# Performance work log

Measured on AMD Instinct MI355X. Metric: run time of the kernel, lower is better.

## Reference

```python
import jax, jax.numpy as jnp
import numpy as np
import math

B, N = 1, 768
CS, CZ, CH, H, PQ, PV = 384, 128, 16, 12, 4, 8
EPS = 1e-8


def setup_inputs() -> dict:
    key = jax.random.key(0)
    ks = jax.random.split(key, 12)
    def rn(k, shape, scale=1.0):
        return jax.random.normal(k, shape, dtype=jnp.float32) * scale
    s = rn(ks[0], (B, N, CS))
    z = rn(ks[1], (B, N, N, CZ))
    rot, _ = jnp.linalg.qr(rn(ks[2], (B, N, 3, 3)))  # proper-ish rigid rotations
    rot = rot.astype(jnp.float32)
    trans = rn(ks[3], (B, N, 3))
    sc = 0.02
    Wq = rn(ks[4], (CS, H * CH), sc); bq = jnp.zeros((H * CH,), jnp.float32)
    Wkv = rn(ks[5], (CS, 2 * H * CH), sc); bkv = jnp.zeros((2 * H * CH,), jnp.float32)
    Wqp = rn(ks[6], (CS, H * PQ * 3), sc); bqp = jnp.zeros((H * PQ * 3,), jnp.float32)
    Wkvp = rn(ks[7], (CS, H * (PQ + PV) * 3), sc); bkvp = jnp.zeros((H * (PQ + PV) * 3,), jnp.float32)
    Wb = rn(ks[8], (CZ, H), sc); bb = jnp.zeros((H,), jnp.float32)
    head_w = rn(ks[9], (H,), 0.5)
    Wout = rn(ks[10], (H * (CZ + CH + PV * 4), CS), sc); bout = jnp.zeros((CS,), jnp.float32)
    return dict(s=s, z=z, rot=rot, trans=trans, Wq=Wq, bq=bq, Wkv=Wkv, bkv=bkv,
                Wqp=Wqp, bqp=bqp, Wkvp=Wkvp, bkvp=bkvp, Wb=Wb, bb=bb,
                head_w=head_w, Wout=Wout, bout=bout)


def _split_points(x):
    # [B,N,3*M] -> [B,N,M,3]: first M entries are x-coords, next M y, next M z
    return jnp.stack(jnp.split(x, 3, axis=-1), axis=-1)


def _apply_frame(rot, trans, pts):
    # pts [B,N,M,3] -> R @ p + t
    return jnp.einsum('bnxy,bnmy->bnmx', rot, pts) + trans[:, :, None, :]


def reference(s, z, rot, trans, Wq, bq, Wkv, bkv, Wqp, bqp, Wkvp, bkvp, Wb, bb, head_w, Wout, bout):
    # scalar q/k/v: [B,N,H,CH]
    q = (s @ Wq + bq).reshape(B, N, H, CH)
    kv = (s @ Wkv + bkv).reshape(B, N, H, 2 * CH)
    k, v = kv[..., :CH], kv[..., CH:]

    # point q/k/v in global frame
    q_pts = _apply_frame(rot, trans, _split_points(s @ Wqp + bqp)).reshape(B, N, H, PQ, 3)
    kv_pts = _apply_frame(rot, trans, _split_points(s @ Wkvp + bkvp)).reshape(B, N, H, PQ + PV, 3)
    k_pts, v_pts = kv_pts[..., :PQ, :], kv_pts[..., PQ:, :]

    # pair bias [B,N,N,H]
    b = z @ Wb + bb

    # scalar attention logits [B,H,i,j]
    a = jnp.einsum('bihc,bjhc->bhij', q, k) * math.sqrt(1.0 / (3 * CH))
    a = a + math.sqrt(1.0 / 3) * jnp.transpose(b, (0, 3, 1, 2))

    # point-distance attention: [B,i,j,H,PQ]
    diff = q_pts[:, :, None] - k_pts[:, None]          # [B,i,j,H,PQ,3]
    d2 = jnp.sum(diff * diff, axis=-1)                  # [B,i,j,H,PQ]
    hw = jax.nn.softplus(head_w) * math.sqrt(1.0 / (3 * (PQ * 9.0 / 2)))
    pt_att = -0.5 * jnp.sum(d2 * hw[None, None, None, :, None], axis=-1)  # [B,i,j,H]
    a = a + jnp.transpose(pt_att, (0, 3, 1, 2))

    a = jax.nn.softmax(a, axis=-1)                      # [B,H,i,j]

    # scalar output [B,N,H*CH]
    o = jnp.einsum('bhij,bjhc->bihc', a, v).reshape(B, N, H * CH)

    # point output [B,i,H,PV,3], mapped back into local frame of residue i
    o_pt = jnp.einsum('bhij,bjhpx->bihpx', a, v_pts)
    o_pt = jnp.einsum('bnyx,bnhpy->bnhpx', rot, o_pt - trans[:, :, None, None, :])
    o_pt_norm = jnp.sqrt(jnp.sum(o_pt * o_pt, axis=-1) + EPS).reshape(B, N, H * PV)
    o_pt_flat = o_pt.reshape(B, N, H * PV, 3)

    # pair output [B,N,H*CZ]
    o_pair = jnp.einsum('bhij,bijc->bihc', a, z).reshape(B, N, H * CZ)

    cat = jnp.concatenate(
        [o, o_pt_flat[..., 0], o_pt_flat[..., 1], o_pt_flat[..., 2], o_pt_norm, o_pair], axis=-1)
    return cat @ Wout + bout
```

## Files before the change

kernel.cpp:

```cpp
#include <hip/hip_runtime.h>
#include <hip/hip_bf16.h>
#include <cmath>

#define NN 768
#define CS 384
#define CZ 128
#define CH 16
#define HH 12
#define PQ 4
#define PV 8
#define CATC 2112

typedef __attribute__((ext_vector_type(8))) __bf16 bf16x8;
typedef __attribute__((ext_vector_type(8))) unsigned short us8;
typedef __attribute__((ext_vector_type(4))) float f32x4;

__device__ __forceinline__ unsigned short f2bf(float f) {
  unsigned int u = __builtin_bit_cast(unsigned int, f);
  u += 0x7FFFu + ((u >> 16) & 1u);
  return (unsigned short)(u >> 16);
}
__device__ __forceinline__ float bf2f(unsigned short u) {
  return __builtin_bit_cast(float, ((unsigned int)u) << 16);
}
__device__ __forceinline__ unsigned short nf2bf(float f) {
  __bf16 b = (__bf16)f;
  return __builtin_bit_cast(unsigned short, b);
}

__global__ void k_proj(const float* __restrict__ s, const float* __restrict__ rot,
                       const float* __restrict__ trans,
                       const float* __restrict__ Wq, const float* __restrict__ bq,
                       const float* __restrict__ Wkv, const float* __restrict__ bkv,
                       const float* __restrict__ Wqp, const float* __restrict__ bqp,
                       const float* __restrict__ Wkvp, const float* __restrict__ bkvp,
                       float* __restrict__ q, float* __restrict__ kk, float* __restrict__ vv,
                       float* __restrict__ qpts, float* __restrict__ kvpts) {
  __shared__ float srow[CS];
  __shared__ float rawq[144];
  __shared__ float rawkv[432];
  __shared__ float R[9];
  __shared__ float T[3];
  int n = blockIdx.x, t = threadIdx.x;
  for (int u = t; u < CS; u += 256) srow[u] = s[(size_t)n*CS + u];
  if (t < 9) R[t] = rot[(size_t)n*9 + t];
  if (t < 3) T[t] = trans[(size_t)n*3 + t];
  __syncthreads();

  for (int col = t; col < 192; col += 256) {
    float acc = bq[col];
    for (int c = 0; c < CS; c++) acc += srow[c] * Wq[(size_t)c*192 + col];
    q[(size_t)n*192 + col] = acc;
  }
  for (int col = t; col < 384; col += 256) {
    float acc = bkv[col];
    for (int c = 0; c < CS; c++) acc += srow[c] * Wkv[(size_t)c*384 + col];
    int h = col >> 5, u2 = col & 31;
    if (u2 < 16) kk[(size_t)n*192 + h*16 + u2] = acc;
    else         vv[(size_t)n*192 + h*16 + (u2-16)] = acc;
  }
  for (int col = t; col < 144; col += 256) {
    float acc = bqp[col];
    for (int c = 0; c < CS; c++) acc += srow[c] * Wqp[(size_t)c*144 + col];
    rawq[col] = acc;
  }
  for (int col = t; col < 432; col += 256) {
    float acc = bkvp[col];
    for (int c = 0; c < CS; c++) acc += srow[c] * Wkvp[(size_t)c*432 + col];
    rawkv[col] = acc;
  }
  __syncthreads();

  for (int u = t; u < 48*3; u += 256) {
    int m = u / 3, x = u % 3;
    float p0 = rawq[0*48 + m], p1 = rawq[1*48 + m], p2 = rawq[2*48 + m];
    qpts[((size_t)n*48 + m)*3 + x] = R[x*3+0]*p0 + R[x*3+1]*p1 + R[x*3+2]*p2 + T[x];
  }
  for (int u = t; u < 144*3; u += 256) {
    int m = u / 3, x = u % 3;
    float p0 = rawkv[0*144 + m], p1 = rawkv[1*144 + m], p2 = rawkv[2*144 + m];
    kvpts[((size_t)n*144 + m)*3 + x] = R[x*3+0]*p0 + R[x*3+1]*p1 + R[x*3+2]*p2 + T[x];
  }
}

__global__ void k_prep_all(const float* __restrict__ kk, const float* __restrict__ kvpts,
                           const float* __restrict__ Wb, const float* __restrict__ q,
                           const float* __restrict__ qpts, const float* __restrict__ bb,
                           const float* __restrict__ head_w, const float* __restrict__ vv,
                           unsigned short* __restrict__ Bq, unsigned short* __restrict__ afT,
                           unsigned short* __restrict__ augT, unsigned short* __restrict__ Vq) {
  int b = blockIdx.x, t = threadIdx.x;
  if (b < 48) {
    int jt16 = b;
    for (int u = t; u < 768; u += 256) {
      int hp = u >> 6, kg = (u >> 4) & 3, l15 = u & 15;
      int j = jt16*16 + l15;
      unsigned short vals[8];
      #pragma unroll
      for (int e = 0; e < 8; e++) {
        int cc = kg*8 + e;
        float v;
        if (cc < 16) {
          v = kk[(size_t)j*192 + hp*16 + cc];
        } else if (cc < 28) {
          v = kvpts[(size_t)j*432 + hp*36 + (cc-16)];
        } else if (cc == 28) {
          float s2 = 0.f;
          #pragma unroll
          for (int m = 0; m < 12; m++) {
            float d = kvpts[(size_t)j*432 + hp*36 + m];
            s2 += d*d;
          }
          v = s2;
        } else if (cc == 29) {
          v = 1.0f;
        } else {
          v = 0.f;
        }
        vals[e] = f2bf(v);
      }
      *(us8*)(Bq + ((size_t)(jt16*12 + hp)*64 + kg*16 + l15)*8) = *(const us8*)vals;
    }
    if (b == 0) {
      int kg = t >> 6, l15 = (t >> 2) & 15, ks = t & 3;
      unsigned short vals[8];
      #pragma unroll
      for (int kc = 0; kc < 8; kc++) {
        vals[kc] = (l15 < 12)
          ? f2bf(0.5773502691896258f * Wb[(size_t)(ks*32 + kg*8 + kc)*12 + l15])
          : (unsigned short)0;
      }
      *(us8*)(afT + (size_t)t*8) = *(const us8*)vals;
    }
  } else if (b < 240) {
    int g = (b-48)*256 + t;
    int i = g >> 6, kg = (g >> 4) & 3, l15 = g & 15;
    const float sc1 = 0.14433756729740643f;
    const float sc3 = 0.5773502691896258f;
    float hw = (l15 < 12) ? log1pf(expf(head_w[l15])) * 0.13608276348795434f : 0.f;
    unsigned short vals[8];
    #pragma unroll
    for (int e = 0; e < 8; e++) {
      int idx = kg*8 + e;
      float v = 0.f;
      if (l15 < 12) {
        if (idx < 16) v = sc1 * q[(size_t)i*192 + l15*16 + idx];
        else if (idx < 28) v = hw * qpts[(size_t)i*144 + l15*12 + (idx-16)];
        else if (idx == 28) v = -0.5f * hw;
        else if (idx == 29) {
          float s2 = 0.f;
          #pragma unroll
          for (int m = 0; m < 12; m++) {
            float d = qpts[(size_t)i*144 + l15*12 + m];
            s2 += d*d;
          }
          v = sc3 * bb[l15] - 0.5f * hw * s2;
        }
      }
      vals[e] = f2bf(v);
    }
    *(us8*)(augT + (size_t)g*8) = *(const us8*)vals;
  } else {
    int g = (b-240)*256 + t;
    int l15 = g & 15;
    int kg  = (g >> 4) & 3;
    int r2  = g >> 6;
    int ks  = r2 % 24;
    int hn  = r2 / 24;
    int nt  = hn % 3;
    int h   = hn / 3;
    int col = nt*16 + l15;
    unsigned short vals[8];
    #pragma unroll
    for (int e = 0; e < 8; e++) {
      int j = ks*32 + kg*8 + e;
      float v = 0.f;
      if (col < 16)      v = vv[(size_t)j*192 + h*16 + col];
      else if (col < 40) v = kvpts[(size_t)j*432 + h*36 + 12 + (col-16)];
      vals[e] = f2bf(v);
    }
    *(us8*)(Vq + (size_t)g*8) = *(const us8*)vals;
  }
}

#define PL2 136
__global__ void __launch_bounds__(512) k_zpass(
    const float* __restrict__ z, const unsigned short* __restrict__ Bq,
    const unsigned short* __restrict__ afT, const unsigned short* __restrict__ augT,
    unsigned short* __restrict__ p_bf, float* __restrict__ Pp,
    float* __restrict__ msbuf) {
  __shared__ unsigned short zt[128*128];
  __shared__ unsigned short p_l[16*PL2];
  __shared__ float redm[8][16];
  __shared__ float reds[8][16];
  int jt = blockIdx.x, i = blockIdx.y, t = threadIdx.x;
  int w = t >> 6, l = t & 63, kg = l >> 4, l15 = l & 15;
  const us8* afT8 = (const us8*)afT;
  const us8* augT8 = (const us8*)augT;
  const us8* Bq8 = (const us8*)Bq;
  us8 zero8 = {0,0,0,0,0,0,0,0};

  us8 af[4];
  #pragma unroll
  for (int ks = 0; ks < 4; ks++) af[ks] = afT8[(kg*16 + l15)*4 + ks];
  us8 aug = augT8[((size_t)i*4 + kg)*16 + l15];

  int jloc = w*16 + l15;
  int jcol = jt*128 + jloc;
  const float* zr = z + ((size_t)i*NN + jcol)*CZ;
  f32x4 accz = {0.f,0.f,0.f,0.f};
  f32x4 aa0 = {0.f,0.f,0.f,0.f}, aa1 = {0.f,0.f,0.f,0.f}, aa2 = {0.f,0.f,0.f,0.f};
  #pragma unroll
  for (int ks = 0; ks < 4; ks++) {
    float4 z0 = *(const float4*)(zr + ks*32 + kg*8);
    float4 z1 = *(const float4*)(zr + ks*32 + kg*8 + 4);
    bf16x8 bv;
    bv[0] = (__bf16)z0.x; bv[1] = (__bf16)z0.y; bv[2] = (__bf16)z0.z; bv[3] = (__bf16)z0.w;
    bv[4] = (__bf16)z1.x; bv[5] = (__bf16)z1.y; bv[6] = (__bf16)z1.z; bv[7] = (__bf16)z1.w;
    us8 bu = __builtin_bit_cast(us8, bv);
    #pragma unroll
    for (int e = 0; e < 8; e++) {
      int c = ks*32 + kg*8 + e;
      int js = (jloc + 16*((c>>3)&3) + 8*(c&7)) & 127;
      zt[c*128 + js] = bu[e];
    }
    accz = __builtin_amdgcn_mfma_f32_16x16x32_bf16(
        __builtin_bit_cast(bf16x8, af[ks]), bv, accz, 0, 0, 0);
  }
  int jtile = jt*8 + w;
  #pragma unroll
  for (int hp = 0; hp < 12; hp++) {
    us8 bqv = Bq8[(size_t)(jtile*12 + hp)*64 + kg*16 + l15];
    us8 sel = (l15 == hp) ? aug : zero8;
    f32x4* dst = (hp < 4) ? &aa0 : (hp < 8) ? &aa1 : &aa2;
    *dst = __builtin_amdgcn_mfma_f32_16x16x32_bf16(
        __builtin_bit_cast(bf16x8, sel), __builtin_bit_cast(bf16x8, bqv), *dst, 0, 0, 0);
  }
  f32x4 lg = (accz + aa0) + (aa1 + aa2);

  float mr[4];
  #pragma unroll
  for (int r = 0; r < 4; r++) {
    float m = lg[r];
    #pragma unroll
    for (int off = 1; off < 16; off <<= 1) m = fmaxf(m, __shfl_xor(m, off));
    mr[r] = m;
  }
  if (l15 == 0) {
    #pragma unroll
    for (int r = 0; r < 4; r++) redm[w][kg*4+r] = mr[r];
  }
  __syncthreads();
  float er[4], mloc[4], sr[4];
  #pragma unroll
  for (int r = 0; r < 4; r++) {
    int h = kg*4 + r;
    float m = redm[0][h];
    #pragma unroll
    for (int ww = 1; ww < 8; ww++) m = fmaxf(m, redm[ww][h]);
    mloc[r] = m;
    float e = expf(lg[r] - m);
    er[r] = e;
    float s = e;
    #pragma unroll
    for (int off = 1; off < 16; off <<= 1) s += __shfl_xor(s, off);
    sr[r] = s;
  }
  if (l15 == 0) {
    #pragma unroll
    for (int r = 0; r < 4; r++) reds[w][kg*4+r] = sr[r];
  }
  #pragma unroll
  for (int r = 0; r < 4; r++) {
    int row = kg*4 + r;
    p_l[row*PL2 + jloc] = (kg < 3) ? nf2bf(er[r]) : (unsigned short)0;
  }
  __syncthreads();
  if (w == 0 && l15 == 0 && kg < 3) {
    #pragma unroll
    for (int r = 0; r < 4; r++) {
      int h = kg*4 + r;
      float s_loc = reds[0][h] + reds[1][h] + reds[2][h] + reds[3][h]
                  + reds[4][h] + reds[5][h] + reds[6][h] + reds[7][h];
      msbuf[((size_t)i*6 + jt)*24 + h]      = mloc[r];
      msbuf[((size_t)i*6 + jt)*24 + 12 + h] = s_loc;
    }
  }

  {
    const us8* pl8 = (const us8*)p_l;
    us8* pg8 = (us8*)(p_bf + (size_t)i*12*768);
    if (t < 192) {
      int h = t >> 4, c8 = t & 15;
      pg8[h*96 + jt*16 + c8] = pl8[h*17 + c8];
    }
  }

  {
    const us8* pl8 = (const us8*)p_l;
    f32x4 acc = {0.f,0.f,0.f,0.f};
    int c = w*16 + l15;
    int off = 16*((c>>3)&3) + 8*(c&7);
    #pragma unroll
    for (int ks = 0; ks < 4; ks++) {
      us8 av = pl8[l15*17 + ks*4 + kg];
      us8 b = *(const us8*)(zt + c*128 + ((ks*32 + kg*8 + off) & 127));
      acc = __builtin_amdgcn_mfma_f32_16x16x32_bf16(
          __builtin_bit_cast(bf16x8, av), __builtin_bit_cast(bf16x8, b), acc, 0, 0, 0);
    }
    #pragma unroll
    for (int r = 0; r < 4; r++) {
      int h = kg*4 + r;
      if (h < 12)
        Pp[(((size_t)i*6 + jt)*12 + h)*128 + c] = acc[r];
    }
  }
}

__global__ void k_comb(const float* __restrict__ Pp, const float* __restrict__ msbuf,
                       unsigned short* __restrict__ p_bf, float* __restrict__ cat) {
  __shared__ float alpha[12][6];
  int i = blockIdx.x, t = threadIdx.x;
  if (t < 12) {
    int h = t;
    float ml[6];
    float m = -1e30f;
    #pragma unroll
    for (int jt = 0; jt < 6; jt++) {
      ml[jt] = msbuf[((size_t)i*6 + jt)*24 + h];
      m = fmaxf(m, ml[jt]);
    }
    float s = 0.f;
    float al[6];
    #pragma unroll
    for (int jt = 0; jt < 6; jt++) {
      al[jt] = expf(ml[jt] - m);
      s += msbuf[((size_t)i*6 + jt)*24 + 12 + h] * al[jt];
    }
    float invs = 1.0f / s;
    #pragma unroll
    for (int jt = 0; jt < 6; jt++) alpha[h][jt] = al[jt] * invs;
  }
  __syncthreads();
  for (int u = t; u < 1536; u += 256) {
    int h = u >> 7, c = u & 127;
    float acc = 0.f;
    #pragma unroll
    for (int jt = 0; jt < 6; jt++)
      acc += Pp[(((size_t)i*6 + jt)*12 + h)*128 + c] * alpha[h][jt];
    cat[(size_t)i*CATC + 576 + h*128 + c] = acc;
  }
  us8* pg8 = (us8*)(p_bf + (size_t)i*12*768);
  for (int u = t; u < 1152; u += 256) {
    int h = u / 96, c8 = u % 96, jt = c8 >> 4;
    float a = alpha[h][jt];
    us8 v = pg8[h*96 + c8];
    #pragma unroll
    for (int e = 0; e < 8; e++) v[e] = nf2bf(bf2f(v[e]) * a);
    pg8[h*96 + c8] = v;
  }
}

__global__ void k_ov(const unsigned short* __restrict__ p_bf,
                     const unsigned short* __restrict__ Vq,
                     const float* __restrict__ rot, const float* __restrict__ trans,
                     float* __restrict__ cat) {
  __shared__ float opt[16][28];
  __shared__ float Rl[16][9];
  __shared__ float Tl[16][3];
  int it = blockIdx.x, h = blockIdx.y, t = threadIdx.x;
  int i0 = it*16;
  int w = t >> 6, l = t & 63, kg = l >> 4, l15 = l & 15;
  if (t < 144) Rl[t/9][t%9] = rot[(size_t)(i0 + t/9)*9 + (t%9)];
  if (t >= 192 && t < 240) {
    int u = t - 192;
    Tl[u/3][u%3] = trans[(size_t)(i0 + u/3)*3 + (u%3)];
  }
  f32x4 acc = {0.f,0.f,0.f,0.f};
  if (w < 3) {
    const unsigned short* prow = p_bf + ((size_t)(i0 + l15)*12 + h)*768 + kg*8;
    const us8* vq = (const us8*)Vq + (size_t)(h*3 + w)*24*64 + kg*16 + l15;
    for (int ks = 0; ks < 24; ks++) {
      us8 av = *(const us8*)(prow + ks*32);
      us8 bv = vq[(size_t)ks*64];
      acc = __builtin_amdgcn_mfma_f32_16x16x32_bf16(
          __builtin_bit_cast(bf16x8, av), __builtin_bit_cast(bf16x8, bv), acc, 0, 0, 0);
    }
  }
  if (w == 0) {
    #pragma unroll
    for (int r = 0; r < 4; r++)
      cat[(size_t)(i0 + kg*4 + r)*CATC + h*16 + l15] = acc[r];
  } else if (w == 1) {
    #pragma unroll
    for (int r = 0; r < 4; r++) opt[kg*4 + r][l15] = acc[r];
  } else if (w == 2) {
    if (l15 < 8) {
      #pragma unroll
      for (int r = 0; r < 4; r++) opt[kg*4 + r][16 + l15] = acc[r];
    }
  }
  __syncthreads();
  if (t < 128) {
    int ip = t >> 3, p = t & 7;
    float x0 = opt[ip][p*3+0] - Tl[ip][0];
    float x1 = opt[ip][p*3+1] - Tl[ip][1];
    float x2 = opt[ip][p*3+2] - Tl[ip][2];
    const float* R = Rl[ip];
    float ox = R[0]*x0 + R[3]*x1 + R[6]*x2;
    float oy = R[1]*x0 + R[4]*x1 + R[7]*x2;
    float oz = R[2]*x0 + R[5]*x1 + R[8]*x2;
    float nrm = sqrtf(ox*ox + oy*oy + oz*oz + 1e-8f);
    float* c = cat + (size_t)(i0 + ip)*CATC;
    int m = h*8 + p;
    c[192 + m] = ox; c[288 + m] = oy; c[384 + m] = oz; c[480 + m] = nrm;
  }
}

#define OROWS 3
__global__ void k_out(const float* __restrict__ cat, const float* __restrict__ Wout,
                      const float* __restrict__ bout, float* __restrict__ out) {
  __shared__ float cl[OROWS*CATC];
  int i0 = blockIdx.x*OROWS, t = threadIdx.x;
  for (int idx = t; idx < OROWS*CATC; idx += 384) cl[idx] = cat[(size_t)i0*CATC + idx];
  __syncthreads();
  float acc[OROWS];
  #pragma unroll
  for (int g = 0; g < OROWS; g++) acc[g] = 0.f;
  for (int r = 0; r < CATC; r += 8) {
    float wv[8];
    #pragma unroll
    for (int u = 0; u < 8; u++) wv[u] = Wout[(size_t)(r+u)*384 + t];
    #pragma unroll
    for (int u = 0; u < 8; u++) {
      #pragma unroll
      for (int g = 0; g < OROWS; g++) acc[g] += cl[g*CATC + r + u] * wv[u];
    }
  }
  float bo = bout[t];
  #pragma unroll
  for (int g = 0; g < OROWS; g++) out[(size_t)(i0+g)*384 + t] = acc[g] + bo;
}

extern "C" void kernel_launch(void* const* d_in, const int* in_sizes, int n_in,
                              void* d_out, int out_size, void* d_ws, size_t ws_size,
                              hipStream_t stream) {
  const float* s      = (const float*)d_in[0];
  const float* z      = (const float*)d_in[1];
  const float* rot    = (const float*)d_in[2];
  const float* trans  = (const float*)d_in[3];
  const float* Wq     = (const float*)d_in[4];
  const float* bq     = (const float*)d_in[5];
  const float* Wkv    = (const float*)d_in[6];
  const float* bkv    = (const float*)d_in[7];
  const float* Wqp    = (const float*)d_in[8];
  const float* bqp    = (const float*)d_in[9];
  const float* Wkvp   = (const float*)d_in[10];
  const float* bkvp   = (const float*)d_in[11];
  const float* Wb     = (const float*)d_in[12];
  const float* bb     = (const float*)d_in[13];
  const float* head_w = (const float*)d_in[14];
  const float* Wout   = (const float*)d_in[15];
  const float* bout   = (const float*)d_in[16];
  float* out = (float*)d_out;

  float* ws    = (float*)d_ws;
  float* q     = ws;
  float* kk    = q     + 147456;
  float* vv    = kk    + 147456;
  float* qpts  = vv    + 147456;
  float* kvpts = qpts  + 110592;
  unsigned short* p_bf = (unsigned short*)(kvpts + 331776);
  float* cat   = (float*)(p_bf + 7077888);
  unsigned short* Bq  = (unsigned short*)(cat + 1622016);
  unsigned short* Vq  = Bq + 294912;
  unsigned short* afT = Vq + 884736;
  unsigned short* augT= afT + 2048;
  float* Pp    = (float*)(augT + 393216);
  float* msbuf = Pp + 7077888;

  k_proj<<<768, 256, 0, stream>>>(s, rot, trans, Wq, bq, Wkv, bkv, Wqp, bqp,
                                  Wkvp, bkvp, q, kk, vv, qpts, kvpts);
  k_prep_all<<<672, 256, 0, stream>>>(kk, kvpts, Wb, q, qpts, bb, head_w, vv,
                                      Bq, afT, augT, Vq);
  k_zpass<<<dim3(6, 768), 512, 0, stream>>>(z, Bq, afT, augT, p_bf, Pp, msbuf);
  k_comb<<<768, 256, 0, stream>>>(Pp, msbuf, p_bf, cat);
  k_ov<<<dim3(48, 12), 256, 0, stream>>>(p_bf, Vq, rot, trans, cat);
  k_out<<<256, 384, 0, stream>>>(cat, Wout, bout, out);
}
```

Before: 301.5 us.

## Batch projection over 8 rows with concatenated weights; bf16 Wout for output GEMM

Replaces the per-row projection kernel with one where each block handles 8 residues. A new prep kernel first concatenates Wq/Wkv/Wqp/Wkvp into a single 1152-wide matrix, so each weight load is reused across 8 rows instead of one. The same prep kernel converts Wout to bf16, which halves the weight traffic in the output GEMM at some precision cost. It adds an extra kernel launch plus a weight copy on every call, and the projection now runs on only 96 blocks.

After: 303.4 us, median of 2. Within noise of the previous version (+0.6%).

```diff
diff --git a/kernel.cpp b/kernel.cpp
--- a/kernel.cpp
+++ b/kernel.cpp
@@ -28,58 +28,131 @@
   return __builtin_bit_cast(unsigned short, b);
 }
 
-__global__ void k_proj(const float* __restrict__ s, const float* __restrict__ rot,
-                       const float* __restrict__ trans,
-                       const float* __restrict__ Wq, const float* __restrict__ bq,
-                       const float* __restrict__ Wkv, const float* __restrict__ bkv,
-                       const float* __restrict__ Wqp, const float* __restrict__ bqp,
-                       const float* __restrict__ Wkvp, const float* __restrict__ bkvp,
-                       float* __restrict__ q, float* __restrict__ kk, float* __restrict__ vv,
-                       float* __restrict__ qpts, float* __restrict__ kvpts) {
-  __shared__ float srow[CS];
-  __shared__ float rawq[144];
-  __shared__ float rawkv[432];
-  __shared__ float R[9];
-  __shared__ float T[3];
-  int n = blockIdx.x, t = threadIdx.x;
-  for (int u = t; u < CS; u += 256) srow[u] = s[(size_t)n*CS + u];
-  if (t < 9) R[t] = rot[(size_t)n*9 + t];
-  if (t < 3) T[t] = trans[(size_t)n*3 + t];
-  __syncthreads();
-
-  for (int col = t; col < 192; col += 256) {
-    float acc = bq[col];
-    for (int c = 0; c < CS; c++) acc += srow[c] * Wq[(size_t)c*192 + col];
-    q[(size_t)n*192 + col] = acc;
-  }
-  for (int col = t; col < 384; col += 256) {
-    float acc = bkv[col];
-    for (int c = 0; c < CS; c++) acc += srow[c] * Wkv[(size_t)c*384 + col];
-    int h = col >> 5, u2 = col & 31;
-    if (u2 < 16) kk[(size_t)n*192 + h*16 + u2] = acc;
-    else         vv[(size_t)n*192 + h*16 + (u2-16)] = acc;
-  }
-  for (int col = t; col < 144; col += 256) {
-    float acc = bqp[col];
-    for (int c = 0; c < CS; c++) acc += srow[c] * Wqp[(size_t)c*144 + col];
-    rawq[col] = acc;
-  }
-  for (int col = t; col < 432; col += 256) {
-    float acc = bkvp[col];
-    for (int c = 0; c < CS; c++) acc += srow[c] * Wkvp[(size_t)c*432 + col];
-    rawkv[col] = acc;
-  }
-  __syncthreads();
-
-  for (int u = t; u < 48*3; u += 256) {
-    int m = u / 3, x = u % 3;
-    float p0 = rawq[0*48 + m], p1 = rawq[1*48 + m], p2 = rawq[2*48 + m];
-    qpts[((size_t)n*48 + m)*3 + x] = R[x*3+0]*p0 + R[x*3+1]*p1 + R[x*3+2]*p2 + T[x];
-  }
-  for (int u = t; u < 144*3; u += 256) {
-    int m = u / 3, x = u % 3;
-    float p0 = rawkv[0*144 + m], p1 = rawkv[1*144 + m], p2 = rawkv[2*144 + m];
-    kvpts[((size_t)n*144 + m)*3 + x] = R[x*3+0]*p0 + R[x*3+1]*p1 + R[x*3+2]*p2 + T[x];
+__global__ void k_prep_w(const float* __restrict__ Wq, const float* __restrict__ Wkv,
+                         const float* __restrict__ Wqp, const float* __restrict__ Wkvp,
+                         const float* __restrict__ Wout,
+                         float* __restrict__ Wall, unsigned short* __restrict__ Wout_bf) {
+  int g = blockIdx.x*256 + threadIdx.x;
+  if (g < 442368) {
+    int c = g / 1152, col = g % 1152;
+    float v;
+    if (col < 192)      v = Wq[(size_t)c*192 + col];
+    else if (col < 576) v = Wkv[(size_t)c*384 + (col-192)];
+    else if (col < 720) v = Wqp[(size_t)c*144 + (col-576)];
+    else                v = Wkvp[(size_t)c*432 + (col-720)];
+    Wall[g] = v;
+  } else {
+    int g2 = g - 442368;
+    if (g2 < 811008) Wout_bf[g2] = nf2bf(Wout[g2]);
+  }
+}
+
+__global__ void __launch_bounds__(384) k_projg(
+    const float* __restrict__ s, const float* __restrict__ Wall,
+    const float* __restrict__ rot, const float* __restrict__ trans,
+    const float* __restrict__ bq, const float* __restrict__ bkv,
+    const float* __restrict__ bqp, const float* __restrict__ bkvp,
+    float* __restrict__ q, float* __restrict__ kk, float* __restrict__ vv,
+    float* __restrict__ qpts, float* __restrict__ kvpts) {
+  __shared__ float sl[8][384];
+  __shared__ float raw[8][576];
+  __shared__ float Rl[8][9];
+  __shared__ float Tl[8][3];
+  int i0 = blockIdx.x*8, t = threadIdx.x;
+  #pragma unroll
+  for (int k = 0; k < 8; k++) sl[k][t] = s[(size_t)(i0+k)*CS + t];
+  if (t < 72) Rl[t/9][t%9] = rot[(size_t)i0*9 + t];
+  else if (t < 96) { int u = t-72; Tl[u/3][u%3] = trans[(size_t)i0*3 + u]; }
+  __syncthreads();
+
+  float a0[8], a1[8], a2[8];
+  #pragma unroll
+  for (int g = 0; g < 8; g++) { a0[g]=0.f; a1[g]=0.f; a2[g]=0.f; }
+  {
+    const float* w0 = Wall + t;
+    const float* w1 = Wall + 384 + t;
+    const float* w2 = Wall + 768 + t;
+    #pragma unroll 4
+    for (int c4 = 0; c4 < 96; c4++) {
+      float4 sv[8];
+      #pragma unroll
+      for (int g = 0; g < 8; g++) sv[g] = *(const float4*)&sl[g][c4*4];
+      #pragma unroll
+      for (int e = 0; e < 4; e++) {
+        int c = c4*4 + e;
+        float wv0 = w0[(size_t)c*1152];
+        float wv1 = w1[(size_t)c*1152];
+        float wv2 = w2[(size_t)c*1152];
+        #pragma unroll
+        for (int g = 0; g < 8; g++) {
+          float svv = (e==0)?sv[g].x:(e==1)?sv[g].y:(e==2)?sv[g].z:sv[g].w;
+          a0[g] += svv*wv0; a1[g] += svv*wv1; a2[g] += svv*wv2;
+        }
+      }
+    }
+  }
+  if (t < 192) {
+    float b = bq[t];
+    #pragma unroll
+    for (int g = 0; g < 8; g++) q[(size_t)(i0+g)*192 + t] = a0[g] + b;
+  } else {
+    int cc = t - 192;
+    float b = bkv[cc];
+    int h = cc >> 5, u2 = cc & 31;
+    #pragma unroll
+    for (int g = 0; g < 8; g++) {
+      float v = a0[g] + b;
+      if (u2 < 16) kk[(size_t)(i0+g)*192 + h*16 + u2] = v;
+      else         vv[(size_t)(i0+g)*192 + h*16 + (u2-16)] = v;
+    }
+  }
+  if (t < 192) {
+    int cc = t + 192;
+    float b = bkv[cc];
+    int h = cc >> 5, u2 = cc & 31;
+    #pragma unroll
+    for (int g = 0; g < 8; g++) {
+      float v = a1[g] + b;
+      if (u2 < 16) kk[(size_t)(i0+g)*192 + h*16 + u2] = v;
+      else         vv[(size_t)(i0+g)*192 + h*16 + (u2-16)] = v;
+    }
+  } else if (t < 336) {
+    int m = t - 192;
+    float b = bqp[m];
+    #pragma unroll
+    for (int g = 0; g < 8; g++) raw[g][m] = a1[g] + b;
+  } else {
+    int m2 = t - 336;
+    float b = bkvp[m2];
+    #pragma unroll
+    for (int g = 0; g < 8; g++) raw[g][144 + m2] = a1[g] + b;
+  }
+  {
+    int m2 = t + 48;
+    float b = bkvp[m2];
+    #pragma unroll
+    for (int g = 0; g < 8; g++) raw[g][144 + m2] = a2[g] + b;
+  }
+  __syncthreads();
+
+  for (int u = t; u < 8*192; u += 384) {
+    int g = u / 192, pt = u % 192;
+    const float* R = Rl[g];
+    const float* T = Tl[g];
+    if (pt < 48) {
+      float p0 = raw[g][pt], p1 = raw[g][48+pt], p2 = raw[g][96+pt];
+      float* d = qpts + ((size_t)(i0+g)*48 + pt)*3;
+      d[0] = R[0]*p0 + R[1]*p1 + R[2]*p2 + T[0];
+      d[1] = R[3]*p0 + R[4]*p1 + R[5]*p2 + T[1];
+      d[2] = R[6]*p0 + R[7]*p1 + R[8]*p2 + T[2];
+    } else {
+      int m = pt - 48;
+      float p0 = raw[g][144+m], p1 = raw[g][288+m], p2 = raw[g][432+m];
+      float* d = kvpts + ((size_t)(i0+g)*144 + m)*3;
+      d[0] = R[0]*p0 + R[1]*p1 + R[2]*p2 + T[0];
+      d[1] = R[3]*p0 + R[4]*p1 + R[5]*p2 + T[1];
+      d[2] = R[6]*p0 + R[7]*p1 + R[8]*p2 + T[2];
+    }
   }
 }
 
@@ -418,7 +491,7 @@
 }
 
 #define OROWS 3
-__global__ void k_out(const float* __restrict__ cat, const float* __restrict__ Wout,
+__global__ void k_out(const float* __restrict__ cat, const unsigned short* __restrict__ Wout_bf,
                       const float* __restrict__ bout, float* __restrict__ out) {
   __shared__ float cl[OROWS*CATC];
   int i0 = blockIdx.x*OROWS, t = threadIdx.x;
@@ -430,7 +503,7 @@
   for (int r = 0; r < CATC; r += 8) {
     float wv[8];
     #pragma unroll
-    for (int u = 0; u < 8; u++) wv[u] = Wout[(size_t)(r+u)*384 + t];
+    for (int u = 0; u < 8; u++) wv[u] = bf2f(Wout_bf[(size_t)(r+u)*384 + t]);
     #pragma unroll
     for (int u = 0; u < 8; u++) {
       #pragma unroll
@@ -478,13 +551,16 @@
   unsigned short* augT= afT + 2048;
   float* Pp    = (float*)(augT + 393216);
   float* msbuf = Pp + 7077888;
-
-  k_proj<<<768, 256, 0, stream>>>(s, rot, trans, Wq, bq, Wkv, bkv, Wqp, bqp,
-                                  Wkvp, bkvp, q, kk, vv, qpts, kvpts);
+  float* Wall  = msbuf + 110592;
+  unsigned short* Wout_bf = (unsigned short*)(Wall + 442368);
+
+  k_prep_w<<<4896, 256, 0, stream>>>(Wq, Wkv, Wqp, Wkvp, Wout, Wall, Wout_bf);
+  k_projg<<<96, 384, 0, stream>>>(s, Wall, rot, trans, bq, bkv, bqp, bkvp,
+                                  q, kk, vv, qpts, kvpts);
   k_prep_all<<<672, 256, 0, stream>>>(kk, kvpts, Wb, q, qpts, bb, head_w, vv,
                                       Bq, afT, augT, Vq);
   k_zpass<<<dim3(6, 768), 512, 0, stream>>>(z, Bq, afT, augT, p_bf, Pp, msbuf);
   k_comb<<<768, 256, 0, stream>>>(Pp, msbuf, p_bf, cat);
   k_ov<<<dim3(48, 12), 256, 0, stream>>>(p_bf, Vq, rot, trans, cat);
-  k_out<<<256, 384, 0, stream>>>(cat, Wout, bout, out);
-}
+  k_out<<<256, 384, 0, stream>>>(cat, Wout_bf, bout, out);
+}
```
